# Performance work log

Hardware: AMD Instinct MI355X
Metric: run time of the kernel (lower is better)

Reference implementation:

```python
import jax, jax.numpy as jnp
import numpy as np

V, E, B, NODES_PER_GRAPH = 100000, 128, 4096, 64
N = B * NODES_PER_GRAPH  # 262144 nodes per side
EPS = 1e-6


def setup_inputs() -> dict:
    key = jax.random.key(0)
    k1, k2, k3, k4, k5, k6 = jax.random.split(key, 6)
    left_x = jax.random.randint(k1, (N, 1), 0, V, dtype=jnp.int64 if jax.config.jax_enable_x64 else jnp.int32)
    right_x = jax.random.randint(k2, (N, 1), 0, V, dtype=left_x.dtype)
    # sorted segment ids with every graph non-empty (64 nodes per graph)
    batch_ids = jnp.repeat(jnp.arange(B, dtype=left_x.dtype), NODES_PER_GRAPH)
    label = jax.random.randint(k3, (B,), 0, 2).astype(jnp.float32)
    emb_table = jax.random.normal(k4, (V, E), dtype=jnp.float32)
    W = jax.random.normal(k5, (E, E), dtype=jnp.float32) / np.sqrt(E)
    b = jax.random.normal(k6, (E,), dtype=jnp.float32) * 0.01
    return {
        "left_x": left_x,
        "left_graph_index": jnp.arange(B, dtype=left_x.dtype),
        "right_x": right_x,
        "right_graph_index": jnp.arange(B, dtype=left_x.dtype),
        "left_x_batch": batch_ids,
        "right_x_batch": batch_ids,
        "label": label,
        "emb_table": emb_table,
        "W": W,
        "b": b,
    }


def _side_emb(x, x_batch, emb_table, W, b, num_segments):
    node_emb = emb_table[x[:, 0]]                       # [N, E] gather
    pooled = jax.ops.segment_max(node_emb, x_batch,      # [B, E] scatter-max
                                 num_segments=num_segments,
                                 indices_are_sorted=True)
    return pooled @ W.T + b                              # trans_linear


def reference(left_x, left_graph_index, right_x, right_graph_index,
              left_x_batch, right_x_batch, label, emb_table, W, b):
    num_segments = label.shape[0]
    left_final = _side_emb(left_x, left_x_batch, emb_table, W, b, num_segments)
    right_final = _side_emb(right_x, right_x_batch, emb_table, W, b, num_segments)
    # torch CosineSimilarity(eps=1e-6): clamp each norm at eps
    dot = jnp.sum(left_final * right_final, axis=-1)
    nl = jnp.maximum(jnp.linalg.norm(left_final, axis=-1), EPS)
    nr = jnp.maximum(jnp.linalg.norm(right_final, axis=-1), EPS)
    cos = dot / (nl * nr)                                # [B]
    # ContrastiveLoss(margin=1.0), size_average=True
    losses = 0.5 * ((1.0 - label) * cos ** 2
                    + label * jnp.maximum(1.0 - cos, 0.0) ** 2)
    sim_loss = losses.mean()
    return sim_loss, cos
```

## Files before the change

kernel.cpp:

```cpp
#include <hip/hip_runtime.h>
#include <math.h>

#define B_GRAPHS 4096
#define NPG 64
#define E_DIM 128
#define INV_B (1.0f / 4096.0f)

static __device__ __forceinline__ float4 fmax4(float4 a, float4 b) {
    return make_float4(fmaxf(a.x, b.x), fmaxf(a.y, b.y),
                       fmaxf(a.z, b.z), fmaxf(a.w, b.w));
}

__global__ __launch_bounds__(256) void fused_graph_sim_k(
    const int* __restrict__ lx, const int* __restrict__ rx,
    const float* __restrict__ emb, const float* __restrict__ W,
    const float* __restrict__ bias, const float* __restrict__ label,
    float* __restrict__ out)
{
    const int g    = blockIdx.x;
    const int t    = threadIdx.x;
    const int w    = t >> 6;
    const int lane = t & 63;

    __shared__ int    idxs[2][NPG];
    __shared__ float  rows[NPG][E_DIM];
    __shared__ float4 part[4][32];
    __shared__ float4 P4[2][32];
    __shared__ float  wred[3][4];

    if (t < NPG)          idxs[0][t]       = lx[g * NPG + t];
    else if (t < 2 * NPG) idxs[1][t - NPG] = rx[g * NPG + (t - NPG)];
    __syncthreads();

    const int q     = lane & 31;
    const int rbase = w * 16;

    #pragma unroll
    for (int side = 0; side < 2; ++side) {
        #pragma unroll
        for (int j = 0; j < 8; ++j) {
            const int r = rbase + 2 * j + (lane >> 5);
            const float* gsrc =
                emb + (size_t)idxs[side][r] * E_DIM + q * 4;
            __builtin_amdgcn_global_load_lds(
                (const __attribute__((address_space(1))) void*)gsrc,
                (__attribute__((address_space(3))) void*)&rows[rbase + 2 * j][0],
                16, 0, 0);
        }
        asm volatile("s_waitcnt vmcnt(0)" ::: "memory");
        __syncthreads();

        float4 m = make_float4(-INFINITY, -INFINITY, -INFINITY, -INFINITY);
        #pragma unroll
        for (int k = 0; k < 8; ++k) {
            const int r = rbase + 2 * k + (lane >> 5);
            m = fmax4(m, *reinterpret_cast<const float4*>(&rows[r][q * 4]));
        }
        m.x = fmaxf(m.x, __shfl_xor(m.x, 32));
        m.y = fmaxf(m.y, __shfl_xor(m.y, 32));
        m.z = fmaxf(m.z, __shfl_xor(m.z, 32));
        m.w = fmaxf(m.w, __shfl_xor(m.w, 32));
        if (lane < 32) part[w][q] = m;
        __syncthreads();

        if (t < 32)
            P4[side][t] = fmax4(fmax4(part[0][t], part[1][t]),
                                fmax4(part[2][t], part[3][t]));
        __syncthreads();
    }

    float acc;
    {
        const int side = t & 1;
        const int e    = t >> 1;
        acc = bias[e];
        const float4* __restrict__ wr =
            reinterpret_cast<const float4*>(W) + (size_t)e * 32;
        const float4* __restrict__ pv = P4[side];
        #pragma unroll 8
        for (int fi = 0; fi < 32; ++fi) {
            const float4 wv = wr[fi];
            const float4 p  = pv[fi];
            acc = fmaf(p.x, wv.x, acc);
            acc = fmaf(p.y, wv.y, acc);
            acc = fmaf(p.z, wv.z, acc);
            acc = fmaf(p.w, wv.w, acc);
        }
    }

    {
        const float other = __shfl_xor(acc, 1);
        const float l = (t & 1) ? other : acc;
        const float r = (t & 1) ? acc   : other;
        float dot = l * r;
        float nl  = l * l;
        float nr  = r * r;
        #pragma unroll
        for (int off = 1; off < 64; off <<= 1) {
            dot += __shfl_xor(dot, off);
            nl  += __shfl_xor(nl,  off);
            nr  += __shfl_xor(nr,  off);
        }
        if (lane == 0) {
            wred[0][w] = dot; wred[1][w] = nl; wred[2][w] = nr;
        }
    }
    __syncthreads();

    if (t == 0) {
        const float dd = 0.5f * (wred[0][0] + wred[0][1] + wred[0][2] + wred[0][3]);
        const float ll = 0.5f * (wred[1][0] + wred[1][1] + wred[1][2] + wred[1][3]);
        const float rr = 0.5f * (wred[2][0] + wred[2][1] + wred[2][2] + wred[2][3]);
        const float nlv = fmaxf(sqrtf(ll), 1e-6f);
        const float nrv = fmaxf(sqrtf(rr), 1e-6f);
        const float c   = dd / (nlv * nrv);
        out[1 + g] = c;
        const float lab  = label[g];
        const float mm   = fmaxf(1.0f - c, 0.0f);
        const float loss = 0.5f * ((1.0f - lab) * c * c + lab * mm * mm);
        atomicAdd(out, loss * INV_B);
    }
}

extern "C" void kernel_launch(void* const* d_in, const int* in_sizes, int n_in,
                              void* d_out, int out_size, void* d_ws, size_t ws_size,
                              hipStream_t stream)
{
    const int*   lx    = (const int*)d_in[0];
    const int*   rx    = (const int*)d_in[2];
    const float* label = (const float*)d_in[6];
    const float* emb   = (const float*)d_in[7];
    const float* W     = (const float*)d_in[8];
    const float* bias  = (const float*)d_in[9];

    float* out = (float*)d_out;

    hipMemsetAsync(out, 0, sizeof(float), stream);

    fused_graph_sim_k<<<B_GRAPHS, 256, 0, stream>>>(
        lx, rx, emb, W, bias, label, out);
}
```

Before: 164.5 us.

## Split fused kernel into gather-pool kernel and matvec-cosine kernel

Splits the single fused kernel into two launches. The first, a 2D grid over graph and side, gathers embedding rows straight into registers with float4 loads and max-pools them, then writes the pooled vectors to workspace. The second reads the pooled vectors back and does the linear layer, cosine similarity and loss. The intent is to drop the 32KB LDS staging buffer and its barriers so more blocks can be resident and more gathers stay in flight. The cost is an extra launch and a round trip of the pooled data through global memory.

```diff
diff --git a/kernel.cpp b/kernel.cpp
--- a/kernel.cpp
+++ b/kernel.cpp
@@ -11,9 +11,59 @@
                        fmaxf(a.z, b.z), fmaxf(a.w, b.w));
 }
 
-__global__ __launch_bounds__(256) void fused_graph_sim_k(
+__global__ __launch_bounds__(256) void gather_pool_k(
     const int* __restrict__ lx, const int* __restrict__ rx,
-    const float* __restrict__ emb, const float* __restrict__ W,
+    const float* __restrict__ emb, float* __restrict__ pooled)
+{
+    const int g    = blockIdx.x;
+    const int side = blockIdx.y;
+    const int t    = threadIdx.x;
+    const int w    = t >> 6;
+    const int lane = t & 63;
+
+    __shared__ int   idx[NPG];
+    __shared__ float red[4][E_DIM];
+
+    const int* __restrict__ x = side ? rx : lx;
+    if (t < NPG) idx[t] = x[g * NPG + t];
+    __syncthreads();
+
+    const int n0 = t >> 5;
+    const int q  = t & 31;
+    const float4* __restrict__ e4 = reinterpret_cast<const float4*>(emb);
+
+    float4 a = make_float4(-INFINITY, -INFINITY, -INFINITY, -INFINITY);
+    #pragma unroll
+    for (int i = 0; i < 8; ++i)
+        a = fmax4(a, e4[(size_t)idx[(i << 3) + n0] * 32 + q]);
+
+    a.x = fmaxf(a.x, __shfl_xor(a.x, 32));
+    a.y = fmaxf(a.y, __shfl_xor(a.y, 32));
+    a.z = fmaxf(a.z, __shfl_xor(a.z, 32));
+    a.w = fmaxf(a.w, __shfl_xor(a.w, 32));
+
+    if (lane < 32) {
+        const int o = w * 32 + lane;
+        red[0][o] = a.x; red[1][o] = a.y; red[2][o] = a.z; red[3][o] = a.w;
+    }
+    __syncthreads();
+
+    if (t < 32) {
+        float4 m;
+        m.x = fmaxf(fmaxf(red[0][t],      red[0][32 + t]),
+                    fmaxf(red[0][64 + t], red[0][96 + t]));
+        m.y = fmaxf(fmaxf(red[1][t],      red[1][32 + t]),
+                    fmaxf(red[1][64 + t], red[1][96 + t]));
+        m.z = fmaxf(fmaxf(red[2][t],      red[2][32 + t]),
+                    fmaxf(red[2][64 + t], red[2][96 + t]));
+        m.w = fmaxf(fmaxf(red[3][t],      red[3][32 + t]),
+                    fmaxf(red[3][64 + t], red[3][96 + t]));
+        reinterpret_cast<float4*>(pooled)[((size_t)side * B_GRAPHS + g) * 32 + t] = m;
+    }
+}
+
+__global__ __launch_bounds__(256) void matvec_cos_k(
+    const float* __restrict__ pooled, const float* __restrict__ W,
     const float* __restrict__ bias, const float* __restrict__ label,
     float* __restrict__ out)
 {
@@ -22,52 +72,16 @@
     const int w    = t >> 6;
     const int lane = t & 63;
 
-    __shared__ int    idxs[2][NPG];
-    __shared__ float  rows[NPG][E_DIM];
-    __shared__ float4 part[4][32];
     __shared__ float4 P4[2][32];
     __shared__ float  wred[3][4];
 
-    if (t < NPG)          idxs[0][t]       = lx[g * NPG + t];
-    else if (t < 2 * NPG) idxs[1][t - NPG] = rx[g * NPG + (t - NPG)];
+    if (t < 64) {
+        const int side = t >> 5;
+        const int qq   = t & 31;
+        P4[side][qq] = reinterpret_cast<const float4*>(pooled)
+            [((size_t)side * B_GRAPHS + g) * 32 + qq];
+    }
     __syncthreads();
-
-    const int q     = lane & 31;
-    const int rbase = w * 16;
-
-    #pragma unroll
-    for (int side = 0; side < 2; ++side) {
-        #pragma unroll
-        for (int j = 0; j < 8; ++j) {
-            const int r = rbase + 2 * j + (lane >> 5);
-            const float* gsrc =
-                emb + (size_t)idxs[side][r] * E_DIM + q * 4;
-            __builtin_amdgcn_global_load_lds(
-                (const __attribute__((address_space(1))) void*)gsrc,
-                (__attribute__((address_space(3))) void*)&rows[rbase + 2 * j][0],
-                16, 0, 0);
-        }
-        asm volatile("s_waitcnt vmcnt(0)" ::: "memory");
-        __syncthreads();
-
-        float4 m = make_float4(-INFINITY, -INFINITY, -INFINITY, -INFINITY);
-        #pragma unroll
-        for (int k = 0; k < 8; ++k) {
-            const int r = rbase + 2 * k + (lane >> 5);
-            m = fmax4(m, *reinterpret_cast<const float4*>(&rows[r][q * 4]));
-        }
-        m.x = fmaxf(m.x, __shfl_xor(m.x, 32));
-        m.y = fmaxf(m.y, __shfl_xor(m.y, 32));
-        m.z = fmaxf(m.z, __shfl_xor(m.z, 32));
-        m.w = fmaxf(m.w, __shfl_xor(m.w, 32));
-        if (lane < 32) part[w][q] = m;
-        __syncthreads();
-
-        if (t < 32)
-            P4[side][t] = fmax4(fmax4(part[0][t], part[1][t]),
-                                fmax4(part[2][t], part[3][t]));
-        __syncthreads();
-    }
 
     float acc;
     {
@@ -133,10 +147,12 @@
     const float* W     = (const float*)d_in[8];
     const float* bias  = (const float*)d_in[9];
 
-    float* out = (float*)d_out;
+    float* out    = (float*)d_out;
+    float* pooled = (float*)d_ws;
 
     hipMemsetAsync(out, 0, sizeof(float), stream);
 
-    fused_graph_sim_k<<<B_GRAPHS, 256, 0, stream>>>(
-        lx, rx, emb, W, bias, label, out);
+    dim3 gA(B_GRAPHS, 2);
+    gather_pool_k<<<gA, 256, 0, stream>>>(lx, rx, emb, pooled);
+    matvec_cos_k<<<B_GRAPHS, 256, 0, stream>>>(pooled, W, bias, label, out);
 }
```

Measured after the change: 191.4 us. 16.3% more time.
